# Kernel optimization log

Hardware: AMD Instinct MI355X
Metric: run time of the kernel (lower is better)

The kernel has to match this reference:

```python
import jax, jax.numpy as jnp
import numpy as np

BOARD = 19
TOKENS = BOARD * BOARD          # 361
C = 512
H = 8
DH = C // H                     # 64
MLP = 2048
SPAN = 2 * BOARD - 1            # 37
TABLE = SPAN * SPAN             # 1369
EPS = 1e-6


def _relative_position_index(board_size):
    coords = np.arange(board_size, dtype=np.int32)
    row, col = np.meshgrid(coords, coords, indexing='ij')
    flat = np.stack((row.reshape(-1), col.reshape(-1)), axis=1)
    rel = flat[:, None, :] - flat[None, :, :]
    span = 2 * board_size - 1
    return (rel[..., 0] + board_size - 1) * span + (rel[..., 1] + board_size - 1)


REL_INDEX = jnp.asarray(_relative_position_index(BOARD))  # [T, T] int32


def _layernorm(x, scale, bias):
    mu = jnp.mean(x, axis=-1, keepdims=True)
    var = jnp.mean(jnp.square(x - mu), axis=-1, keepdims=True)
    return (x - mu) * jax.lax.rsqrt(var + EPS) * scale + bias


def setup_inputs() -> dict:
    key = jax.random.key(0)
    ks = jax.random.split(key, 12)
    B = 256
    s = lambda k, shape, sc: jax.random.normal(k, shape, dtype=jnp.float32) * sc
    return {
        'x': s(ks[0], (B, TOKENS, C), 1.0),
        'ln1_scale': jnp.ones((C,), jnp.float32),
        'ln1_bias': jnp.zeros((C,), jnp.float32),
        'Wq': s(ks[1], (C, H, DH), C ** -0.5),
        'bq': jnp.zeros((H, DH), jnp.float32),
        'Wk': s(ks[2], (C, H, DH), C ** -0.5),
        'bk': jnp.zeros((H, DH), jnp.float32),
        'Wv': s(ks[3], (C, H, DH), C ** -0.5),
        'bv': jnp.zeros((H, DH), jnp.float32),
        'Wo': s(ks[4], (C, C), C ** -0.5),
        'bo': jnp.zeros((C,), jnp.float32),
        'rel_pos_bias': s(ks[5], (H, TABLE), 0.02),
        'ln2_scale': jnp.ones((C,), jnp.float32),
        'ln2_bias': jnp.zeros((C,), jnp.float32),
        'W1': s(ks[6], (C, MLP), C ** -0.5),
        'b1': jnp.zeros((MLP,), jnp.float32),
        'W2': s(ks[7], (MLP, C), MLP ** -0.5),
        'b2': jnp.zeros((C,), jnp.float32),
    }


def reference(x, ln1_scale, ln1_bias, Wq, bq, Wk, bk, Wv, bv, Wo, bo,
              rel_pos_bias, ln2_scale, ln2_bias, W1, b1, W2, b2):
    # --- attention ---
    y = _layernorm(x, ln1_scale, ln1_bias)
    q = jnp.einsum('btc,chd->bthd', y, Wq) + bq
    k = jnp.einsum('btc,chd->bthd', y, Wk) + bk
    v = jnp.einsum('btc,chd->bthd', y, Wv) + bv
    logits = jnp.einsum('bthd,bshd->bhts', q, k) * jnp.float32(DH ** -0.5)
    rel_bias = jnp.take(rel_pos_bias, REL_INDEX.reshape(-1), axis=1)
    rel_bias = rel_bias.reshape(H, TOKENS, TOKENS)          # [H, T, T]
    logits = logits + rel_bias[None]
    attn = jax.nn.softmax(logits.astype(jnp.float32), axis=-1).astype(x.dtype)
    ctx = jnp.einsum('bhts,bshd->bthd', attn, v)
    ctx = ctx.reshape(ctx.shape[0], ctx.shape[1], C)
    x = x + ctx @ Wo + bo
    # --- MLP ---
    y = _layernorm(x, ln2_scale, ln2_bias)
    y = jax.nn.gelu(y @ W1 + b1, approximate=True)
    return x + y @ W2 + b2
```

## Files before the change

kernel.cpp:

```cpp
#include <hip/hip_runtime.h>
#include <hip/hip_bf16.h>

#define TOKENS 361
#define CDIM 512
#define NHEAD 8
#define DHEAD 64
#define MLPDIM 2048
#define BATCH 256
#define NTOK (BATCH * TOKENS)
#define HTOK (NTOK / 2)
#define SPAN 37
#define QKVSTR 1536

typedef unsigned int uint32;

typedef __attribute__((ext_vector_type(8))) short bf16x8;
typedef __attribute__((ext_vector_type(4))) float f32x4;

__device__ __forceinline__ unsigned short f2bfu(float f) {
  union { float f; uint32 i; } c; c.f = f;
  uint32 i = c.i;
  uint32 r = (i + 0x7fffu + ((i >> 16) & 1u)) >> 16;
  return (unsigned short)r;
}
__device__ __forceinline__ float bfu2f(unsigned short u) {
  union { uint32 i; float f; } c; c.i = ((uint32)u) << 16; return c.f;
}
__device__ __forceinline__ float lo2f(uint32 u) {
  union { uint32 i; float f; } c; c.i = u << 16; return c.f;
}
__device__ __forceinline__ float hi2f(uint32 u) {
  union { uint32 i; float f; } c; c.i = u & 0xffff0000u; return c.f;
}

__device__ __forceinline__ void gload16(const void* g, void* l) {
  __builtin_amdgcn_global_load_lds((const __attribute__((address_space(1))) void*)g,
                                   (__attribute__((address_space(3))) void*)l, 16, 0, 0);
}

__global__ __launch_bounds__(256) void transpose_conv(
    const float* __restrict__ in, unsigned short* __restrict__ out, int R, int Cc) {
  __shared__ float tile[32][33];
  int c0 = blockIdx.x * 32, r0 = blockIdx.y * 32;
  int tx = threadIdx.x & 31, ty = threadIdx.x >> 5;
#pragma unroll
  for (int i = 0; i < 32; i += 8)
    tile[ty + i][tx] = in[(size_t)(r0 + ty + i) * Cc + c0 + tx];
  __syncthreads();
#pragma unroll
  for (int i = 0; i < 32; i += 8)
    out[(size_t)(c0 + ty + i) * R + r0 + tx] = f2bfu(tile[tx][ty + i]);
}

__global__ __launch_bounds__(256) void concat_bias(
    const float* __restrict__ a, const float* __restrict__ b,
    const float* __restrict__ c, float* __restrict__ o) {
  int i = blockIdx.x * 256 + threadIdx.x;
  o[i] = i < 512 ? a[i] : (i < 1024 ? b[i - 512] : c[i - 1024]);
}

__global__ __launch_bounds__(256) void ln_f32(
    const float* __restrict__ x, const float* __restrict__ sc,
    const float* __restrict__ bs, unsigned short* __restrict__ y) {
  int token = blockIdx.x * 4 + (threadIdx.x >> 6);
  int lane = threadIdx.x & 63;
  const float4* xp = (const float4*)(x + (size_t)token * CDIM + lane * 8);
  float4 f0 = xp[0], f1 = xp[1];
  float v[8] = {f0.x, f0.y, f0.z, f0.w, f1.x, f1.y, f1.z, f1.w};
  float sum = 0.f, sumsq = 0.f;
#pragma unroll
  for (int j = 0; j < 8; ++j) { sum += v[j]; sumsq += v[j] * v[j]; }
#pragma unroll
  for (int off = 1; off < 64; off <<= 1) {
    sum += __shfl_xor(sum, off);
    sumsq += __shfl_xor(sumsq, off);
  }
  float mu = sum * (1.f / 512.f);
  float var = sumsq * (1.f / 512.f) - mu * mu;
  float rs = rsqrtf(var + 1e-6f);
  const float4* sp = (const float4*)(sc + lane * 8);
  const float4* bp = (const float4*)(bs + lane * 8);
  float4 s0 = sp[0], s1 = sp[1], b0 = bp[0], b1 = bp[1];
  float sv[8] = {s0.x, s0.y, s0.z, s0.w, s1.x, s1.y, s1.z, s1.w};
  float bv[8] = {b0.x, b0.y, b0.z, b0.w, b1.x, b1.y, b1.z, b1.w};
  uint32 ov[4];
#pragma unroll
  for (int j = 0; j < 4; ++j) {
    float o0 = (v[2 * j] - mu) * rs * sv[2 * j] + bv[2 * j];
    float o1 = (v[2 * j + 1] - mu) * rs * sv[2 * j + 1] + bv[2 * j + 1];
    ov[j] = (uint32)f2bfu(o0) | ((uint32)f2bfu(o1) << 16);
  }
  uint4 outv = {ov[0], ov[1], ov[2], ov[3]};
  *(uint4*)(y + (size_t)token * CDIM + lane * 8) = outv;
}

__global__ __launch_bounds__(256) void ln_bf16(
    const unsigned short* __restrict__ x, const float* __restrict__ sc,
    const float* __restrict__ bs, unsigned short* __restrict__ y) {
  int token = blockIdx.x * 4 + (threadIdx.x >> 6);
  int lane = threadIdx.x & 63;
  uint4 pk = *(const uint4*)(x + (size_t)token * CDIM + lane * 8);
  uint32 uu[4] = {pk.x, pk.y, pk.z, pk.w};
  float v[8];
#pragma unroll
  for (int j = 0; j < 4; ++j) { v[2 * j] = lo2f(uu[j]); v[2 * j + 1] = hi2f(uu[j]); }
  float sum = 0.f, sumsq = 0.f;
#pragma unroll
  for (int j = 0; j < 8; ++j) { sum += v[j]; sumsq += v[j] * v[j]; }
#pragma unroll
  for (int off = 1; off < 64; off <<= 1) {
    sum += __shfl_xor(sum, off);
    sumsq += __shfl_xor(sumsq, off);
  }
  float mu = sum * (1.f / 512.f);
  float var = sumsq * (1.f / 512.f) - mu * mu;
  float rs = rsqrtf(var + 1e-6f);
  const float4* sp = (const float4*)(sc + lane * 8);
  const float4* bp = (const float4*)(bs + lane * 8);
  float4 s0 = sp[0], s1 = sp[1], b0 = bp[0], b1 = bp[1];
  float sv[8] = {s0.x, s0.y, s0.z, s0.w, s1.x, s1.y, s1.z, s1.w};
  float bv[8] = {b0.x, b0.y, b0.z, b0.w, b1.x, b1.y, b1.z, b1.w};
  uint32 ov[4];
#pragma unroll
  for (int j = 0; j < 4; ++j) {
    float o0 = (v[2 * j] - mu) * rs * sv[2 * j] + bv[2 * j];
    float o1 = (v[2 * j + 1] - mu) * rs * sv[2 * j + 1] + bv[2 * j + 1];
    ov[j] = (uint32)f2bfu(o0) | ((uint32)f2bfu(o1) << 16);
  }
  uint4 outv = {ov[0], ov[1], ov[2], ov[3]};
  *(uint4*)(y + (size_t)token * CDIM + lane * 8) = outv;
}

__device__ __forceinline__ float gelu_tanh(float u) {
  float c2 = 0.7978845608028654f * (u + 0.044715f * u * u * u);
  float e = __expf(2.f * c2);
  float th = 1.f - 2.f / (e + 1.f);
  return 0.5f * u * (1.f + th);
}

template <int EPI>
__global__ __launch_bounds__(256) void gemm_bt(
    const unsigned short* __restrict__ A, const unsigned short* __restrict__ BT,
    const float* __restrict__ bias, const float* __restrict__ resf,
    const unsigned short* __restrict__ resb, void* __restrict__ Cc,
    int M, int N, int K, int nbx) {
  __shared__ unsigned short As[128 * 32];
  __shared__ unsigned short Bs[128 * 32];
  int tid = threadIdx.x;
  int wave = tid >> 6, lane = tid & 63;
  int quad = lane >> 4, l16 = lane & 15;

  int nwg = gridDim.x, bid = blockIdx.x;
  int qq = nwg >> 3, rr = nwg & 7;
  int xcd = bid & 7, loc = bid >> 3;
  int L = (xcd < rr ? xcd * (qq + 1) : rr * (qq + 1) + (xcd - rr) * qq) + loc;
  int m0 = (L / nbx) * 128, n0 = (L % nbx) * 128;
  int wm = (wave >> 1) * 64, wn = (wave & 1) * 64;

  f32x4 acc[4][4];
#pragma unroll
  for (int i = 0; i < 4; ++i)
#pragma unroll
    for (int j = 0; j < 4; ++j) acc[i][j] = (f32x4){0.f, 0.f, 0.f, 0.f};

  const unsigned short* gA = A + (size_t)(m0 + (tid >> 2)) * K + (tid & 3) * 8;
  const unsigned short* gA2 = gA + (size_t)64 * K;
  const unsigned short* gB = BT + (size_t)(n0 + (tid >> 2)) * K + (tid & 3) * 8;
  const unsigned short* gB2 = gB + (size_t)64 * K;
  unsigned short* lA0 = As + wave * 512;
  unsigned short* lA1 = As + 2048 + wave * 512;
  unsigned short* lB0 = Bs + wave * 512;
  unsigned short* lB1 = Bs + 2048 + wave * 512;

  for (int k0 = 0; k0 < K; k0 += 32) {
    __syncthreads();
    gload16(gA + k0, lA0);
    gload16(gA2 + k0, lA1);
    gload16(gB + k0, lB0);
    gload16(gB2 + k0, lB1);
    __syncthreads();
    bf16x8 af[4], bfr[4];
#pragma unroll
    for (int mi = 0; mi < 4; ++mi)
      af[mi] = *(const bf16x8*)&As[(wm + mi * 16 + l16) * 32 + quad * 8];
#pragma unroll
    for (int ni = 0; ni < 4; ++ni)
      bfr[ni] = *(const bf16x8*)&Bs[(wn + ni * 16 + l16) * 32 + quad * 8];
#pragma unroll
    for (int mi = 0; mi < 4; ++mi)
#pragma unroll
      for (int ni = 0; ni < 4; ++ni)
        acc[mi][ni] = __builtin_amdgcn_mfma_f32_16x16x32_bf16(af[mi], bfr[ni], acc[mi][ni], 0, 0, 0);
  }

  unsigned short* o16 = (unsigned short*)Cc;
  float* o32 = (float*)Cc;
#pragma unroll
  for (int ni = 0; ni < 4; ++ni) {
    int gc = n0 + wn + ni * 16 + l16;
    float bz = bias[gc];
#pragma unroll
    for (int mi = 0; mi < 4; ++mi) {
#pragma unroll
      for (int r = 0; r < 4; ++r) {
        int gr = m0 + wm + mi * 16 + quad * 4 + r;
        float val = acc[mi][ni][r] + bz;
        if (EPI == 1) val = gelu_tanh(val);
        if (EPI == 2) val += resf[(size_t)gr * N + gc];
        if (EPI == 3) val += bfu2f(resb[(size_t)gr * N + gc]);
        if (EPI == 3) o32[(size_t)gr * N + gc] = val;
        else o16[(size_t)gr * N + gc] = f2bfu(val);
      }
    }
  }
}

#define SROW 72
#define PSTR 392
__global__ __launch_bounds__(256, 1) void attn_mfma(
    const unsigned short* __restrict__ qkv, const float* __restrict__ relb,
    unsigned short* __restrict__ ctx) {
  __shared__ unsigned short Ks[368 * SROW];
  __shared__ unsigned short VT[64 * PSTR];
  __shared__ unsigned short Ps[64 * PSTR];
  __shared__ float biasF[1369];
  int b = blockIdx.x >> 3, h = blockIdx.x & 7;
  int tid = threadIdx.x;
  int wave = tid >> 6, lane = tid & 63;
  int quad = lane >> 4, l16 = lane & 15;
  size_t baseq = ((size_t)b * TOKENS) * QKVSTR + h * DHEAD;
  size_t basec = ((size_t)b * TOKENS) * CDIM + h * DHEAD;
  const unsigned short* kp = qkv + baseq + 512;
  const unsigned short* vp = qkv + baseq + 1024;

  for (int vv = tid; vv < TOKENS * 8; vv += 256) {
    int r = vv >> 3, c = (vv & 7) * 8;
    *(uint4*)&Ks[r * SROW + c] = *(const uint4*)(kp + (size_t)r * QKVSTR + c);
  }
  if (tid < 56) {
    int r = 361 + (tid >> 3), c = (tid & 7) * 8;
    *(uint4*)&Ks[r * SROW + c] = (uint4){0u, 0u, 0u, 0u};
  }
  for (int vv = tid; vv < TOKENS * 8; vv += 256) {
    int s = vv >> 3, c = (vv & 7) * 8;
    uint4 pk = *(const uint4*)(vp + (size_t)s * QKVSTR + c);
    unsigned short* dst = &VT[c * PSTR + s];
    uint32 w0 = pk.x, w1 = pk.y, w2 = pk.z, w3 = pk.w;
    dst[0]        = (unsigned short)w0;  dst[PSTR]     = (unsigned short)(w0 >> 16);
    dst[2 * PSTR] = (unsigned short)w1;  dst[3 * PSTR] = (unsigned short)(w1 >> 16);
    dst[4 * PSTR] = (unsigned short)w2;  dst[5 * PSTR] = (unsigned short)(w2 >> 16);
    dst[6 * PSTR] = (unsigned short)w3;  dst[7 * PSTR] = (unsigned short)(w3 >> 16);
  }
  for (int vv = tid; vv < 64 * 23; vv += 256) {
    int s = 361 + (vv >> 6), d = vv & 63;
    VT[d * PSTR + s] = 0;
  }
  for (int i = tid; i < 1369; i += 256) biasF[i] = relb[h * 1369 + i];
  for (int i = lane; i < 256; i += 64) {
    int rrp = i >> 4, cc = i & 15;
    Ps[(wave * 16 + rrp) * PSTR + 368 + cc] = 0;
  }
  __syncthreads();

  for (int t0 = 0; t0 < TOKENS; t0 += 64) {
    int rowb = t0 + wave * 16;
    const unsigned short* qrow = qkv + baseq + (size_t)(rowb + l16) * QKVSTR + quad * 8;
    bf16x8 aq0 = *(const bf16x8*)(qrow);
    bf16x8 aq1 = *(const bf16x8*)(qrow + 32);
    int tb[4];
#pragma unroll
    for (int r = 0; r < 4; ++r) {
      int t = rowb + quad * 4 + r;
      if (t > 360) t = 360;
      int rt = t / 19, ct = t - rt * 19;
      tb[r] = rt * SPAN + ct + (18 * SPAN + 18);
    }
    f32x4 sc[23];
#pragma unroll
    for (int n = 0; n < 23; ++n) {
      const unsigned short* kr = &Ks[(n * 16 + l16) * SROW + quad * 8];
      bf16x8 b0 = *(const bf16x8*)kr;
      bf16x8 b1 = *(const bf16x8*)(kr + 32);
      f32x4 a = {0.f, 0.f, 0.f, 0.f};
      a = __builtin_amdgcn_mfma_f32_16x16x32_bf16(aq0, b0, a, 0, 0, 0);
      a = __builtin_amdgcn_mfma_f32_16x16x32_bf16(aq1, b1, a, 0, 0, 0);
      sc[n] = a;
    }
    float mx[4] = {-1e30f, -1e30f, -1e30f, -1e30f};
#pragma unroll
    for (int n = 0; n < 23; ++n) {
      int s = n * 16 + l16;
      int sv = s > 360 ? 360 : s;
      int rs = sv / 19, cs = sv - rs * 19;
      int sb = rs * SPAN + cs;
#pragma unroll
      for (int r = 0; r < 4; ++r) {
        float val = sc[n][r] * 0.125f + biasF[tb[r] - sb];
        if (s > 360) val = -1e30f;
        sc[n][r] = val;
        mx[r] = fmaxf(mx[r], val);
      }
    }
#pragma unroll
    for (int off = 1; off < 16; off <<= 1)
#pragma unroll
      for (int r = 0; r < 4; ++r) mx[r] = fmaxf(mx[r], __shfl_xor(mx[r], off));
    float sm[4] = {0.f, 0.f, 0.f, 0.f};
#pragma unroll
    for (int n = 0; n < 23; ++n)
#pragma unroll
      for (int r = 0; r < 4; ++r) {
        float p = __expf(sc[n][r] - mx[r]);
        sc[n][r] = p;
        sm[r] += p;
      }
#pragma unroll
    for (int off = 1; off < 16; off <<= 1)
#pragma unroll
      for (int r = 0; r < 4; ++r) sm[r] += __shfl_xor(sm[r], off);
    float inv[4];
#pragma unroll
    for (int r = 0; r < 4; ++r) inv[r] = 1.f / sm[r];
#pragma unroll
    for (int n = 0; n < 23; ++n)
#pragma unroll
      for (int r = 0; r < 4; ++r)
        Ps[(wave * 16 + quad * 4 + r) * PSTR + n * 16 + l16] = f2bfu(sc[n][r] * inv[r]);
    f32x4 pacc[4];
#pragma unroll
    for (int ni = 0; ni < 4; ++ni) pacc[ni] = (f32x4){0.f, 0.f, 0.f, 0.f};
#pragma unroll
    for (int kk = 0; kk < 12; ++kk) {
      bf16x8 pa = *(const bf16x8*)&Ps[(wave * 16 + l16) * PSTR + kk * 32 + quad * 8];
#pragma unroll
      for (int ni = 0; ni < 4; ++ni) {
        bf16x8 vb = *(const bf16x8*)&VT[(ni * 16 + l16) * PSTR + kk * 32 + quad * 8];
        pacc[ni] = __builtin_amdgcn_mfma_f32_16x16x32_bf16(pa, vb, pacc[ni], 0, 0, 0);
      }
    }
#pragma unroll
    for (int ni = 0; ni < 4; ++ni)
#pragma unroll
      for (int r = 0; r < 4; ++r) {
        int t = rowb + quad * 4 + r;
        if (t < TOKENS)
          ctx[basec + (size_t)t * CDIM + ni * 16 + l16] = f2bfu(pacc[ni][r]);
      }
  }
}

extern "C" void kernel_launch(void* const* d_in, const int* in_sizes, int n_in,
                              void* d_out, int out_size, void* d_ws, size_t ws_size,
                              hipStream_t stream) {
  const float* x     = (const float*)d_in[0];
  const float* ln1_s = (const float*)d_in[1];
  const float* ln1_b = (const float*)d_in[2];
  const float* Wq    = (const float*)d_in[3];
  const float* bq    = (const float*)d_in[4];
  const float* Wk    = (const float*)d_in[5];
  const float* bk    = (const float*)d_in[6];
  const float* Wv    = (const float*)d_in[7];
  const float* bv    = (const float*)d_in[8];
  const float* Wo    = (const float*)d_in[9];
  const float* bo    = (const float*)d_in[10];
  const float* relb  = (const float*)d_in[11];
  const float* ln2_s = (const float*)d_in[12];
  const float* ln2_b = (const float*)d_in[13];
  const float* W1    = (const float*)d_in[14];
  const float* b1    = (const float*)d_in[15];
  const float* W2    = (const float*)d_in[16];
  const float* b2    = (const float*)d_in[17];
  float* out = (float*)d_out;

  char* ws = (char*)d_ws;
  unsigned short* WqT = (unsigned short*)ws;
  unsigned short* WkT = WqT + 512 * 512;
  unsigned short* WvT = WkT + 512 * 512;
  unsigned short* WoT = WvT + 512 * 512;
  unsigned short* W1T = WoT + 512 * 512;
  unsigned short* W2T = W1T + 512 * 2048;
  float* bqkv = (float*)(W2T + 2048 * 512);
  unsigned short* yb  = (unsigned short*)(bqkv + 1536);
  unsigned short* x1b = yb + (size_t)NTOK * CDIM;
  unsigned short* qkvb = x1b + (size_t)NTOK * CDIM;
  unsigned short* ctxb = qkvb + (size_t)HTOK * QKVSTR;
  unsigned short* hdn  = qkvb;

  dim3 blk(256);
  transpose_conv<<<dim3(16, 16), blk, 0, stream>>>(Wq, WqT, 512, 512);
  transpose_conv<<<dim3(16, 16), blk, 0, stream>>>(Wk, WkT, 512, 512);
  transpose_conv<<<dim3(16, 16), blk, 0, stream>>>(Wv, WvT, 512, 512);
  transpose_conv<<<dim3(16, 16), blk, 0, stream>>>(Wo, WoT, 512, 512);
  transpose_conv<<<dim3(64, 16), blk, 0, stream>>>(W1, W1T, 512, 2048);
  transpose_conv<<<dim3(16, 64), blk, 0, stream>>>(W2, W2T, 2048, 512);
  concat_bias<<<dim3(6), blk, 0, stream>>>(bq, bk, bv, bqkv);

  ln_f32<<<NTOK / 4, blk, 0, stream>>>(x, ln1_s, ln1_b, yb);

  for (int c = 0; c < 2; ++c) {
    size_t off = (size_t)c * HTOK;
    const unsigned short* yc = yb + off * CDIM;
    gemm_bt<0><<<dim3(361 * 12), blk, 0, stream>>>(yc, WqT, bqkv, nullptr, nullptr,
                                                   qkvb, HTOK, 1536, 512, 12);
    attn_mfma<<<dim3((BATCH / 2) * NHEAD), blk, 0, stream>>>(qkvb, relb, ctxb);
    gemm_bt<2><<<dim3(361 * 4), blk, 0, stream>>>(ctxb, WoT, bo, x + off * CDIM, nullptr,
                                                  x1b + off * CDIM, HTOK, 512, 512, 4);
  }

  ln_bf16<<<NTOK / 4, blk, 0, stream>>>(x1b, ln2_s, ln2_b, yb);

  for (int c = 0; c < 2; ++c) {
    size_t off = (size_t)c * HTOK;
    gemm_bt<1><<<dim3(361 * 16), blk, 0, stream>>>(yb + off * CDIM, W1T, b1, nullptr, nullptr,
                                                   hdn, HTOK, 2048, 512, 16);
    gemm_bt<3><<<dim3(361 * 4), blk, 0, stream>>>(hdn, W2T, b2, nullptr, x1b + off * CDIM,
                                                  out + off * CDIM, HTOK, 512, 2048, 4);
  }
}
```

Baseline: 1.893 ms.

## Double-buffer GEMM LDS tiles, swizzle LDS chunks, and stage bf16 epilogue through LDS

The bf16 GEMM now keeps two LDS stages for the A and B tiles. It issues the global-to-LDS loads for the next K slice before running the MFMAs on the current one, and needs only one barrier per iteration. The 16-byte chunk positions within each LDS row are XOR-swizzled on both the store and the fragment read, to reduce LDS bank conflicts. For the bf16-output epilogues, results are first written into LDS and then stored to global memory as coalesced 16-byte rows instead of scattered 2-byte stores. The cost is double the LDS footprint, which may reduce occupancy.

```diff
diff --git a/kernel.cpp b/kernel.cpp
--- a/kernel.cpp
+++ b/kernel.cpp
@@ -144,8 +144,7 @@
     const float* __restrict__ bias, const float* __restrict__ resf,
     const unsigned short* __restrict__ resb, void* __restrict__ Cc,
     int M, int N, int K, int nbx) {
-  __shared__ unsigned short As[128 * 32];
-  __shared__ unsigned short Bs[128 * 32];
+  __shared__ unsigned short SH[16384];
   int tid = threadIdx.x;
   int wave = tid >> 6, lane = tid & 63;
   int quad = lane >> 4, l16 = lane & 15;
@@ -163,54 +162,95 @@
 #pragma unroll
     for (int j = 0; j < 4; ++j) acc[i][j] = (f32x4){0.f, 0.f, 0.f, 0.f};
 
-  const unsigned short* gA = A + (size_t)(m0 + (tid >> 2)) * K + (tid & 3) * 8;
+  int srow = tid >> 2;
+  int schunk = ((tid & 3) ^ ((tid >> 3) & 3)) * 8;
+  const unsigned short* gA = A + (size_t)(m0 + srow) * K + schunk;
   const unsigned short* gA2 = gA + (size_t)64 * K;
-  const unsigned short* gB = BT + (size_t)(n0 + (tid >> 2)) * K + (tid & 3) * 8;
+  const unsigned short* gB = BT + (size_t)(n0 + srow) * K + schunk;
   const unsigned short* gB2 = gB + (size_t)64 * K;
-  unsigned short* lA0 = As + wave * 512;
-  unsigned short* lA1 = As + 2048 + wave * 512;
-  unsigned short* lB0 = Bs + wave * 512;
-  unsigned short* lB1 = Bs + 2048 + wave * 512;
-
+
+  {
+    unsigned short* a = SH;
+    unsigned short* bS = SH + 8192;
+    gload16(gA, a + wave * 512);
+    gload16(gA2, a + 2048 + wave * 512);
+    gload16(gB, bS + wave * 512);
+    gload16(gB2, bS + 2048 + wave * 512);
+  }
+  __syncthreads();
+
+  int rq = (quad ^ ((l16 >> 1) & 3)) * 8;
+  int cur = 0;
   for (int k0 = 0; k0 < K; k0 += 32) {
-    __syncthreads();
-    gload16(gA + k0, lA0);
-    gload16(gA2 + k0, lA1);
-    gload16(gB + k0, lB0);
-    gload16(gB2 + k0, lB1);
-    __syncthreads();
+    if (k0 + 32 < K) {
+      int nb = cur ^ 1;
+      unsigned short* a = SH + nb * 4096;
+      unsigned short* bS = SH + 8192 + nb * 4096;
+      gload16(gA + k0 + 32, a + wave * 512);
+      gload16(gA2 + k0 + 32, a + 2048 + wave * 512);
+      gload16(gB + k0 + 32, bS + wave * 512);
+      gload16(gB2 + k0 + 32, bS + 2048 + wave * 512);
+    }
+    const unsigned short* As = SH + cur * 4096;
+    const unsigned short* Bs = SH + 8192 + cur * 4096;
     bf16x8 af[4], bfr[4];
 #pragma unroll
     for (int mi = 0; mi < 4; ++mi)
-      af[mi] = *(const bf16x8*)&As[(wm + mi * 16 + l16) * 32 + quad * 8];
+      af[mi] = *(const bf16x8*)&As[(wm + mi * 16 + l16) * 32 + rq];
 #pragma unroll
     for (int ni = 0; ni < 4; ++ni)
-      bfr[ni] = *(const bf16x8*)&Bs[(wn + ni * 16 + l16) * 32 + quad * 8];
+      bfr[ni] = *(const bf16x8*)&Bs[(wn + ni * 16 + l16) * 32 + rq];
 #pragma unroll
     for (int mi = 0; mi < 4; ++mi)
 #pragma unroll
       for (int ni = 0; ni < 4; ++ni)
         acc[mi][ni] = __builtin_amdgcn_mfma_f32_16x16x32_bf16(af[mi], bfr[ni], acc[mi][ni], 0, 0, 0);
+    __syncthreads();
+    cur ^= 1;
   }
 
   unsigned short* o16 = (unsigned short*)Cc;
   float* o32 = (float*)Cc;
-#pragma unroll
-  for (int ni = 0; ni < 4; ++ni) {
-    int gc = n0 + wn + ni * 16 + l16;
-    float bz = bias[gc];
-#pragma unroll
-    for (int mi = 0; mi < 4; ++mi) {
-#pragma unroll
-      for (int r = 0; r < 4; ++r) {
-        int gr = m0 + wm + mi * 16 + quad * 4 + r;
-        float val = acc[mi][ni][r] + bz;
-        if (EPI == 1) val = gelu_tanh(val);
-        if (EPI == 2) val += resf[(size_t)gr * N + gc];
-        if (EPI == 3) val += bfu2f(resb[(size_t)gr * N + gc]);
-        if (EPI == 3) o32[(size_t)gr * N + gc] = val;
-        else o16[(size_t)gr * N + gc] = f2bfu(val);
-      }
+  if (EPI == 3) {
+#pragma unroll
+    for (int ni = 0; ni < 4; ++ni) {
+      int gc = n0 + wn + ni * 16 + l16;
+      float bz = bias[gc];
+#pragma unroll
+      for (int mi = 0; mi < 4; ++mi) {
+#pragma unroll
+        for (int r = 0; r < 4; ++r) {
+          int gr = m0 + wm + mi * 16 + quad * 4 + r;
+          float val = acc[mi][ni][r] + bz;
+          val += bfu2f(resb[(size_t)gr * N + gc]);
+          o32[(size_t)gr * N + gc] = val;
+        }
+      }
+    }
+  } else {
+#pragma unroll
+    for (int ni = 0; ni < 4; ++ni) {
+      int gc = n0 + wn + ni * 16 + l16;
+      float bz = bias[gc];
+#pragma unroll
+      for (int mi = 0; mi < 4; ++mi) {
+#pragma unroll
+        for (int r = 0; r < 4; ++r) {
+          int lr = wm + mi * 16 + quad * 4 + r;
+          float val = acc[mi][ni][r] + bz;
+          if (EPI == 1) val = gelu_tanh(val);
+          if (EPI == 2) val += resf[(size_t)(m0 + lr) * N + gc];
+          SH[lr * 128 + wn + ni * 16 + l16] = f2bfu(val);
+        }
+      }
+    }
+    __syncthreads();
+    int tg = tid >> 4, t15 = tid & 15;
+#pragma unroll
+    for (int j = 0; j < 8; ++j) {
+      int row = j * 16 + tg;
+      uint4 w = *(const uint4*)&SH[row * 128 + t15 * 8];
+      *(uint4*)(o16 + (size_t)(m0 + row) * N + n0 + t15 * 8) = w;
     }
   }
 }
```

Result: faster. 1.717 ms (-9.3%).
